# Kernel optimization log

Measured on AMD Instinct MI355X. Metric: run time of the kernel, lower is better.

Reference implementation:

```python
import jax, jax.numpy as jnp
import numpy as np

N_SRC, N_DST, N_EDGES = 50000, 50000, 500000
IN_DIM, OUT_DIM, EDGE_DIM = 128, 128, 11
BN_EPS = 1e-5


def setup_inputs() -> dict:
    key = jax.random.key(0)
    ks = jax.random.split(key, 16)
    s = 0.05
    return {
        "src_feat": jax.random.normal(ks[0], (N_SRC, IN_DIM), jnp.float32),
        "dst_feat": jax.random.normal(ks[1], (N_DST, IN_DIM), jnp.float32),
        "edge_feats": jax.random.normal(ks[2], (N_EDGES, EDGE_DIM), jnp.float32),
        "src_idx": jax.random.randint(ks[3], (N_EDGES,), 0, N_SRC, jnp.int32),
        "dst_idx": jax.random.randint(ks[4], (N_EDGES,), 0, N_DST, jnp.int32),
        "W_src": jax.random.normal(ks[5], (IN_DIM, OUT_DIM), jnp.float32) * s,
        "b_src": jnp.zeros((OUT_DIM,), jnp.float32),
        "W_dst": jax.random.normal(ks[6], (IN_DIM, OUT_DIM), jnp.float32) * s,
        "b_dst": jnp.zeros((OUT_DIM,), jnp.float32),
        "W_edge": jax.random.normal(ks[7], (EDGE_DIM, OUT_DIM), jnp.float32) * s,
        "b_edge": jnp.zeros((OUT_DIM,), jnp.float32),
        "attn_w": jax.random.normal(ks[8], (3 * OUT_DIM,), jnp.float32) * s,
        "attn_b": jnp.zeros((), jnp.float32),
        "gamma": jnp.ones((OUT_DIM,), jnp.float32),
        "beta": jnp.zeros((OUT_DIM,), jnp.float32),
        "alpha": jnp.asarray(0.25, jnp.float32),
    }


def reference(src_feat, dst_feat, edge_feats, src_idx, dst_idx,
              W_src, b_src, W_dst, b_dst, W_edge, b_edge,
              attn_w, attn_b, gamma, beta, alpha):
    D = W_src.shape[1]
    # project at node/edge level (math identical to projecting gathered feats)
    hs = src_feat @ W_src + b_src            # [Ns, D]  (linear_src)
    hd = dst_feat @ W_dst + b_dst            # [Nd, D]  (linear_dst)
    ep = edge_feats @ W_edge + b_edge        # [E, D]   (linear_edge)
    # attn_l on concat([src, dst, edge]) == sum of three dot products + bias
    aw_s, aw_d, aw_e = attn_w[:D], attn_w[D:2 * D], attn_w[2 * D:]
    a = (hs @ aw_s)[src_idx] + (hd @ aw_d)[dst_idx] + ep @ aw_e + attn_b  # [E]
    # edge softmax over incoming edges of each dst node
    n_dst = dst_feat.shape[0]
    seg_max = jax.ops.segment_max(a, dst_idx, num_segments=n_dst)
    a_exp = jnp.exp(a - seg_max[dst_idx])
    denom = jax.ops.segment_sum(a_exp, dst_idx, num_segments=n_dst)
    attn = a_exp / denom[dst_idx]            # [E]
    # weighted message = attn * linear_src(src_h); scatter-sum to dst
    msg = attn[:, None] * hs[src_idx]        # [E, D]
    h_new = jax.ops.segment_sum(msg, dst_idx, num_segments=n_dst)  # [Nd, D]
    # BatchNorm1d (training-mode batch statistics)
    mean = jnp.mean(h_new, axis=0)
    var = jnp.var(h_new, axis=0)
    h_bn = (h_new - mean) / jnp.sqrt(var + BN_EPS) * gamma + beta
    # PReLU (single shared alpha); dropout is identity in eval
    return jnp.where(h_bn >= 0, h_bn, alpha * h_bn)
```

## Files before the change

### kernel.cpp

```cpp
#include <hip/hip_runtime.h>
#include <cstddef>

#define NSRC 50000
#define NDST 50000
#define NEDGE 500000
#define DIM 128
#define EDIM 11
#define BN_EPS 1e-5f
#define SCAN_NBLK ((NDST + 255) / 256)

#define HS_BLOCKS ((NSRC + 63) / 64)
#define DS_BLOCKS ((NDST + 31) / 32)
#define ED_BLOCKS ((NEDGE + 1023) / 1024)

typedef short bf16x8 __attribute__((ext_vector_type(8)));
typedef float f32x4 __attribute__((ext_vector_type(4)));

#define OFF_HS      0
#define OFF_SSCORE  (OFF_HS + (size_t)NSRC*DIM)
#define OFF_DSCORE  (OFF_SSCORE + NSRC)
#define OFF_EE      (OFF_DSCORE + NDST)
#define OFF_DEG     (OFF_EE + NEDGE)
#define OFF_COLSUM  (OFF_DEG + NDST)
#define OFF_COLSQ   (OFF_COLSUM + 128)
#define OFF_OFFS    (OFF_COLSQ + 128)
#define OFF_CURSOR  (OFF_OFFS + NDST + 2)
#define OFF_PAIRS   (OFF_CURSOR + NDST)
#define OFF_WDVEC   (OFF_PAIRS + 2*(size_t)NEDGE)
#define OFF_WEVEC   (OFF_WDVEC + 128)
#define OFF_SCAL    (OFF_WEVEC + 16)
#define OFF_PART    (OFF_SCAL + 4)
#define OFF_WT      (((OFF_PART + 256 + 3) / 4) * 4)

__device__ __forceinline__ unsigned short f2bf(float x) {
    unsigned int u = __float_as_uint(x);
    u += 0x7FFFu + ((u >> 16) & 1u);
    return (unsigned short)(u >> 16);
}
__device__ __forceinline__ float bf2f(unsigned int u16) {
    return __uint_as_float(u16 << 16);
}

__global__ void k_prep(const float* __restrict__ W_dst, const float* __restrict__ b_dst,
                       const float* __restrict__ W_edge, const float* __restrict__ b_edge,
                       const float* __restrict__ attn_w, const float* __restrict__ attn_b,
                       float* __restrict__ wd_vec, float* __restrict__ we_vec,
                       float* __restrict__ scal) {
    int t = threadIdx.x;
    float acc = 0.f;
    for (int d = 0; d < DIM; ++d) acc += W_dst[t * DIM + d] * attn_w[DIM + d];
    wd_vec[t] = acc;
    if (t < EDIM) {
        float e = 0.f;
        for (int d = 0; d < DIM; ++d) e += W_edge[t * DIM + d] * attn_w[2 * DIM + d];
        we_vec[t] = e;
    }
    __shared__ float red[128];
    red[t] = b_dst[t] * attn_w[DIM + t];
    __syncthreads();
    for (int s = 64; s > 0; s >>= 1) { if (t < s) red[t] += red[t + s]; __syncthreads(); }
    if (t == 0) scal[0] = red[0];
    __syncthreads();
    red[t] = b_edge[t] * attn_w[2 * DIM + t];
    __syncthreads();
    for (int s = 64; s > 0; s >>= 1) { if (t < s) red[t] += red[t + s]; __syncthreads(); }
    if (t == 0) scal[1] = red[0] + attn_b[0];
}

__global__ __launch_bounds__(256) void k_wt(const float* __restrict__ W,
                                            unsigned short* __restrict__ wt) {
    __shared__ float tile[32][33];
    int bi = blockIdx.x & 3;
    int bj = blockIdx.x >> 2;
    int t = threadIdx.x;
    int cl = t & 31;
    #pragma unroll
    for (int i = 0; i < 4; ++i) {
        int kl = (t >> 5) * 4 + i;
        tile[kl][cl] = W[(size_t)(bi * 32 + kl) * DIM + bj * 32 + cl];
    }
    __syncthreads();
    int ko = t & 31;
    #pragma unroll
    for (int i = 0; i < 4; ++i) {
        int co = (t >> 5) * 4 + i;
        wt[(size_t)(bj * 32 + co) * DIM + bi * 32 + ko] = f2bf(tile[ko][co]);
    }
}

__global__ __launch_bounds__(256) void k_fused(const float* __restrict__ A,
                                               const unsigned short* __restrict__ wt,
                                               const float* __restrict__ bias,
                                               const float* __restrict__ attn_w,
                                               const float* __restrict__ B,
                                               const float* __restrict__ ef,
                                               const int* __restrict__ dst_idx,
                                               const float* __restrict__ wd_vec,
                                               const float* __restrict__ we_vec,
                                               const float* __restrict__ scal,
                                               unsigned short* __restrict__ hsb,
                                               float* __restrict__ s_score,
                                               float* __restrict__ d_score,
                                               float* __restrict__ ee,
                                               int* __restrict__ deg) {
    __shared__ float stage[4][EDIM * 64];
    const int bid = blockIdx.x;
    const int t = threadIdx.x;

    if (bid < HS_BLOCKS) {
        const int wv = t >> 6;
        const int lane = t & 63;
        const int lrow = lane & 15;
        const int kg = lane >> 4;
        const int grow = bid * 64 + wv * 16 + lrow;
        const bool rowok = grow < NSRC;
        const float* arow = A + (size_t)grow * DIM;

        bf16x8 af[4];
        #pragma unroll
        for (int s = 0; s < 4; ++s) {
            float4 p0 = make_float4(0.f, 0.f, 0.f, 0.f), p1 = p0;
            if (rowok) {
                p0 = *reinterpret_cast<const float4*>(arow + 32 * s + kg * 8);
                p1 = *reinterpret_cast<const float4*>(arow + 32 * s + kg * 8 + 4);
            }
            bf16x8 a;
            a[0] = (short)f2bf(p0.x); a[1] = (short)f2bf(p0.y);
            a[2] = (short)f2bf(p0.z); a[3] = (short)f2bf(p0.w);
            a[4] = (short)f2bf(p1.x); a[5] = (short)f2bf(p1.y);
            a[6] = (short)f2bf(p1.z); a[7] = (short)f2bf(p1.w);
            af[s] = a;
        }

        f32x4 acc[8];
        #pragma unroll
        for (int c = 0; c < 8; ++c) acc[c] = (f32x4){0.f, 0.f, 0.f, 0.f};

        #pragma unroll
        for (int c = 0; c < 8; ++c) {
            #pragma unroll
            for (int s = 0; s < 4; ++s) {
                const bf16x8 b = *reinterpret_cast<const bf16x8*>(
                    wt + ((size_t)(16 * c + lrow) * DIM + 32 * s + kg * 8));
                acc[c] = __builtin_amdgcn_mfma_f32_16x16x32_bf16(af[s], b, acc[c], 0, 0, 0);
            }
        }

        float p[4] = {0.f, 0.f, 0.f, 0.f};
        #pragma unroll
        for (int c = 0; c < 8; ++c) {
            float bb = bias[16 * c + lrow];
            float aw = attn_w[16 * c + lrow];
            #pragma unroll
            for (int i = 0; i < 4; ++i) {
                float v = acc[c][i] + bb;
                acc[c][i] = v;
                p[i] += v * aw;
            }
        }
        #pragma unroll
        for (int i = 0; i < 4; ++i) {
            p[i] += __shfl_xor(p[i], 1);
            p[i] += __shfl_xor(p[i], 2);
            p[i] += __shfl_xor(p[i], 4);
            p[i] += __shfl_xor(p[i], 8);
        }
        const int orow0 = bid * 64 + wv * 16 + kg * 4;
        #pragma unroll
        for (int i = 0; i < 4; ++i) {
            int orow = orow0 + i;
            if (orow < NSRC) {
                #pragma unroll
                for (int c = 0; c < 8; ++c)
                    hsb[(size_t)orow * DIM + 16 * c + lrow] = f2bf(acc[c][i]);
                if (lrow == 0) s_score[orow] = p[i];
            }
        }
    } else if (bid < HS_BLOCKS + DS_BLOCKS) {
        int row = (bid - HS_BLOCKS) * 32 + (t >> 3);
        int c0 = (t & 7) * 16;
        if (row >= NDST) return;
        const float4* x = reinterpret_cast<const float4*>(B + (size_t)row * DIM + c0);
        const float4* w = reinterpret_cast<const float4*>(wd_vec + c0);
        float p = 0.f;
        #pragma unroll
        for (int i = 0; i < 4; ++i) {
            float4 a = x[i], b = w[i];
            p += a.x * b.x + a.y * b.y + a.z * b.z + a.w * b.w;
        }
        p += __shfl_xor(p, 1);
        p += __shfl_xor(p, 2);
        p += __shfl_xor(p, 4);
        if ((t & 7) == 0) d_score[row] = p + scal[0];
    } else {
        const int wv = t >> 6;
        const int lane = t & 63;
        float wvv[EDIM];
        #pragma unroll
        for (int k = 0; k < EDIM; ++k) wvv[k] = we_vec[k];
        const float s1 = scal[1];
        const int blkBase = (bid - HS_BLOCKS - DS_BLOCKS) * 1024;

        #pragma unroll
        for (int chunk = 0; chunk < 4; ++chunk) {
            const int e0 = blkBase + wv * 256 + chunk * 64;
            const size_t g0 = (size_t)e0 * EDIM;
            #pragma unroll
            for (int k = 0; k < EDIM; ++k) {
                int j = k * 64 + lane;
                size_t g = g0 + j;
                stage[wv][j] = (g < (size_t)NEDGE * EDIM) ? ef[g] : 0.f;
            }
            __syncthreads();
            int e = e0 + lane;
            if (e < NEDGE) {
                const float* er = &stage[wv][lane * EDIM];
                float a = s1;
                #pragma unroll
                for (int k = 0; k < EDIM; ++k) a += er[k] * wvv[k];
                ee[e] = a;
                atomicAdd(&deg[dst_idx[e]], 1);
            }
            __syncthreads();
        }
    }
}

__global__ __launch_bounds__(256) void k_scanA(const int* __restrict__ deg,
                                               int* __restrict__ off,
                                               int* __restrict__ partials) {
    __shared__ int tmp[256];
    int t = threadIdx.x;
    int i = blockIdx.x * 256 + t;
    int v = (i < NDST) ? deg[i] : 0;
    tmp[t] = v;
    __syncthreads();
    #pragma unroll
    for (int d = 1; d < 256; d <<= 1) {
        int u = (t >= d) ? tmp[t - d] : 0;
        __syncthreads();
        tmp[t] += u;
        __syncthreads();
    }
    if (i < NDST) off[i] = tmp[t] - v;
    if (t == 255) partials[blockIdx.x] = tmp[255];
}

__global__ __launch_bounds__(256) void k_scanB(int* __restrict__ partials) {
    __shared__ int tmp[256];
    int t = threadIdx.x;
    int v = (t < SCAN_NBLK) ? partials[t] : 0;
    tmp[t] = v;
    __syncthreads();
    #pragma unroll
    for (int d = 1; d < 256; d <<= 1) {
        int u = (t >= d) ? tmp[t - d] : 0;
        __syncthreads();
        tmp[t] += u;
        __syncthreads();
    }
    if (t < SCAN_NBLK) partials[t] = tmp[t] - v;
}

__global__ __launch_bounds__(256) void k_scanC(int* __restrict__ off,
                                               int* __restrict__ cursor,
                                               const int* __restrict__ partials) {
    int t = threadIdx.x;
    int i = blockIdx.x * 256 + t;
    if (i < NDST) {
        int f = off[i] + partials[blockIdx.x];
        off[i] = f;
        cursor[i] = f;
    }
    if (i == 0) off[NDST] = NEDGE;
}

__global__ __launch_bounds__(256) void k_scat(const int* __restrict__ src_idx,
                                              const int* __restrict__ dst_idx,
                                              const float* __restrict__ ee,
                                              const float* __restrict__ s_score,
                                              const float* __restrict__ d_score,
                                              int* __restrict__ cursor,
                                              int2* __restrict__ pairs) {
    int base = blockIdx.x * 1024 + threadIdx.x;
    #pragma unroll
    for (int i = 0; i < 4; ++i) {
        int e = base + i * 256;
        if (e < NEDGE) {
            int s = src_idx[e], d = dst_idx[e];
            float w = expf(ee[e] + s_score[s] + d_score[d]);
            int pos = atomicAdd(&cursor[d], 1);
            pairs[pos] = make_int2(s, __float_as_int(w));
        }
    }
}

__global__ __launch_bounds__(256) void k_gather(const unsigned short* __restrict__ hsb,
                                                const int* __restrict__ off,
                                                const int2* __restrict__ pairs,
                                                float* __restrict__ h_new) {
    int wid = (blockIdx.x * blockDim.x + threadIdx.x) >> 6;
    int lane = threadIdx.x & 63;
    if (wid >= NDST) return;
    int b = off[wid], e2 = off[wid + 1];
    int deg = e2 - b;
    float ax = 0.f, ay = 0.f, wsum = 0.f;

    for (int base = 0; base < deg; base += 64) {
        int cnt = min(deg - base, 64);
        int myS = 0;
        float myW = 0.f;
        if (lane < cnt) {
            int2 p = pairs[b + base + lane];
            myS = p.x;
            myW = __int_as_float(p.y);
        }
        wsum += myW;

        int j = 0;
        for (; j + 4 <= cnt; j += 4) {
            int s0 = __shfl(myS, j + 0), s1 = __shfl(myS, j + 1);
            int s2 = __shfl(myS, j + 2), s3 = __shfl(myS, j + 3);
            float w0 = __shfl(myW, j + 0), w1 = __shfl(myW, j + 1);
            float w2 = __shfl(myW, j + 2), w3 = __shfl(myW, j + 3);
            unsigned int v0 = *reinterpret_cast<const unsigned int*>(hsb + (size_t)s0 * DIM + 2 * lane);
            unsigned int v1 = *reinterpret_cast<const unsigned int*>(hsb + (size_t)s1 * DIM + 2 * lane);
            unsigned int v2 = *reinterpret_cast<const unsigned int*>(hsb + (size_t)s2 * DIM + 2 * lane);
            unsigned int v3 = *reinterpret_cast<const unsigned int*>(hsb + (size_t)s3 * DIM + 2 * lane);
            ax += w0 * bf2f(v0 & 0xFFFFu) + w1 * bf2f(v1 & 0xFFFFu)
                + w2 * bf2f(v2 & 0xFFFFu) + w3 * bf2f(v3 & 0xFFFFu);
            ay += w0 * bf2f(v0 >> 16) + w1 * bf2f(v1 >> 16)
                + w2 * bf2f(v2 >> 16) + w3 * bf2f(v3 >> 16);
        }
        for (; j < cnt; ++j) {
            int s0 = __shfl(myS, j);
            float w0 = __shfl(myW, j);
            unsigned int v0 = *reinterpret_cast<const unsigned int*>(hsb + (size_t)s0 * DIM + 2 * lane);
            ax += w0 * bf2f(v0 & 0xFFFFu);
            ay += w0 * bf2f(v0 >> 16);
        }
    }

    #pragma unroll
    for (int m = 1; m < 64; m <<= 1) wsum += __shfl_xor(wsum, m);

    float inv = (deg > 0) ? 1.f / wsum : 0.f;
    reinterpret_cast<float2*>(h_new + (size_t)wid * DIM)[lane] = make_float2(ax * inv, ay * inv);
}

__global__ __launch_bounds__(256) void k_bnstats(const float* __restrict__ h,
                                                 float* __restrict__ colsum,
                                                 float* __restrict__ colsq) {
    int col = threadIdx.x & 127;
    int rp = threadIdx.x >> 7;
    float s = 0.f, q = 0.f;
    for (int r = blockIdx.x * 2 + rp; r < NDST; r += gridDim.x * 2) {
        float x = h[(size_t)r * DIM + col];
        s += x;
        q += x * x;
    }
    __shared__ float ls[2][128], lq[2][128];
    ls[rp][col] = s;
    lq[rp][col] = q;
    __syncthreads();
    if (rp == 0) {
        atomicAdd(&colsum[col], ls[0][col] + ls[1][col]);
        atomicAdd(&colsq[col], lq[0][col] + lq[1][col]);
    }
}

__global__ __launch_bounds__(256) void k_bnfinal(float* __restrict__ h,
                                                 const float* __restrict__ colsum,
                                                 const float* __restrict__ colsq,
                                                 const float* __restrict__ gamma,
                                                 const float* __restrict__ beta,
                                                 const float* __restrict__ alpha_p) {
    const size_t total4 = (size_t)NDST * DIM / 4;
    const float alpha = alpha_p[0];
    const float invN = 1.f / (float)NDST;
    const int c0 = (threadIdx.x & 31) * 4;
    float sc[4], sh[4];
    #pragma unroll
    for (int k = 0; k < 4; ++k) {
        float mean = colsum[c0 + k] * invN;
        float var = colsq[c0 + k] * invN - mean * mean;
        float s = gamma[c0 + k] * rsqrtf(var + BN_EPS);
        sc[k] = s;
        sh[k] = beta[c0 + k] - mean * s;
    }
    size_t stride = (size_t)gridDim.x * blockDim.x;
    for (size_t i = blockIdx.x * blockDim.x + threadIdx.x; i < total4; i += stride) {
        float4 x = reinterpret_cast<float4*>(h)[i];
        float y0 = x.x * sc[0] + sh[0];
        float y1 = x.y * sc[1] + sh[1];
        float y2 = x.z * sc[2] + sh[2];
        float y3 = x.w * sc[3] + sh[3];
        float4 o;
        o.x = y0 >= 0.f ? y0 : alpha * y0;
        o.y = y1 >= 0.f ? y1 : alpha * y1;
        o.z = y2 >= 0.f ? y2 : alpha * y2;
        o.w = y3 >= 0.f ? y3 : alpha * y3;
        reinterpret_cast<float4*>(h)[i] = o;
    }
}

extern "C" void kernel_launch(void* const* d_in, const int* in_sizes, int n_in,
                              void* d_out, int out_size, void* d_ws, size_t ws_size,
                              hipStream_t stream) {
    const float* src_feat   = (const float*)d_in[0];
    const float* dst_feat   = (const float*)d_in[1];
    const float* edge_feats = (const float*)d_in[2];
    const int*   src_idx    = (const int*)d_in[3];
    const int*   dst_idx    = (const int*)d_in[4];
    const float* W_src      = (const float*)d_in[5];
    const float* b_src      = (const float*)d_in[6];
    const float* W_dst      = (const float*)d_in[7];
    const float* b_dst      = (const float*)d_in[8];
    const float* W_edge     = (const float*)d_in[9];
    const float* b_edge     = (const float*)d_in[10];
    const float* attn_w     = (const float*)d_in[11];
    const float* attn_b     = (const float*)d_in[12];
    const float* gamma      = (const float*)d_in[13];
    const float* beta       = (const float*)d_in[14];
    const float* alpha      = (const float*)d_in[15];

    float* ws      = (float*)d_ws;
    unsigned short* hsb = (unsigned short*)(ws + OFF_HS);
    float* s_score = ws + OFF_SSCORE;
    float* d_score = ws + OFF_DSCORE;
    float* ee      = ws + OFF_EE;
    int*   deg     = (int*)(ws + OFF_DEG);
    float* colsum  = ws + OFF_COLSUM;
    float* colsq   = ws + OFF_COLSQ;
    int*   off     = (int*)(ws + OFF_OFFS);
    int*   cursor  = (int*)(ws + OFF_CURSOR);
    int2*  pairs   = (int2*)(ws + OFF_PAIRS);
    float* wd_vec  = ws + OFF_WDVEC;
    float* we_vec  = ws + OFF_WEVEC;
    float* scal    = ws + OFF_SCAL;
    int*   part    = (int*)(ws + OFF_PART);
    unsigned short* wt = (unsigned short*)(ws + OFF_WT);

    float* h_new = (float*)d_out;

    hipMemsetAsync(deg, 0, (NDST + 256) * sizeof(float), stream);

    k_prep<<<1, 128, 0, stream>>>(W_dst, b_dst, W_edge, b_edge, attn_w, attn_b,
                                  wd_vec, we_vec, scal);
    k_wt<<<16, 256, 0, stream>>>(W_src, wt);
    k_fused<<<HS_BLOCKS + DS_BLOCKS + ED_BLOCKS, 256, 0, stream>>>(
        src_feat, wt, b_src, attn_w, dst_feat, edge_feats, dst_idx,
        wd_vec, we_vec, scal, hsb, s_score, d_score, ee, deg);
    k_scanA<<<SCAN_NBLK, 256, 0, stream>>>(deg, off, part);
    k_scanB<<<1, 256, 0, stream>>>(part);
    k_scanC<<<SCAN_NBLK, 256, 0, stream>>>(off, cursor, part);
    k_scat<<<ED_BLOCKS, 256, 0, stream>>>(src_idx, dst_idx, ee, s_score, d_score,
                                          cursor, pairs);
    k_gather<<<(NDST * 64 + 255) / 256, 256, 0, stream>>>(hsb, off, pairs, h_new);
    k_bnstats<<<512, 256, 0, stream>>>(h_new, colsum, colsq);
    k_bnfinal<<<1024, 256, 0, stream>>>(h_new, colsum, colsq, gamma, beta, alpha);
}
```

Before: 163.7 us.

## Pad degree and cursor counters to 64-byte stride, drop LDS staging for edge scores

Degree and cursor counters are spread out so each destination node's counter sits in its own 64-byte slot. The aim is to cut contention on atomics that hit the same cache line. The edge-score path now reads edge features directly from global memory instead of staging them through shared memory, which removes two block barriers per chunk. k_fused also gets a minimum-occupancy hint, and the hs buffer offset is halved to match its bf16 storage. The costs are a much larger counter memset (about 3.2MB each for deg and cursor), strided scan reads, and uncoalesced 44-byte-stride feature loads.

```diff
diff --git a/kernel.cpp b/kernel.cpp
--- a/kernel.cpp
+++ b/kernel.cpp
@@ -16,21 +16,21 @@
 typedef short bf16x8 __attribute__((ext_vector_type(8)));
 typedef float f32x4 __attribute__((ext_vector_type(4)));
 
-#define OFF_HS      0
-#define OFF_SSCORE  (OFF_HS + (size_t)NSRC*DIM)
-#define OFF_DSCORE  (OFF_SSCORE + NSRC)
-#define OFF_EE      (OFF_DSCORE + NDST)
-#define OFF_DEG     (OFF_EE + NEDGE)
-#define OFF_COLSUM  (OFF_DEG + NDST)
-#define OFF_COLSQ   (OFF_COLSUM + 128)
-#define OFF_OFFS    (OFF_COLSQ + 128)
-#define OFF_CURSOR  (OFF_OFFS + NDST + 2)
-#define OFF_PAIRS   (OFF_CURSOR + NDST)
-#define OFF_WDVEC   (OFF_PAIRS + 2*(size_t)NEDGE)
-#define OFF_WEVEC   (OFF_WDVEC + 128)
-#define OFF_SCAL    (OFF_WEVEC + 16)
-#define OFF_PART    (OFF_SCAL + 4)
-#define OFF_WT      (((OFF_PART + 256 + 3) / 4) * 4)
+#define OFF_HS       0
+#define OFF_SSCORE   (OFF_HS + (size_t)NSRC*DIM/2)
+#define OFF_DSCORE   (OFF_SSCORE + NSRC)
+#define OFF_EE       (OFF_DSCORE + NDST)
+#define OFF_DEG16    (OFF_EE + NEDGE)
+#define OFF_COLSUM   (OFF_DEG16 + (size_t)NDST*16)
+#define OFF_COLSQ    (OFF_COLSUM + 128)
+#define OFF_OFFS     (OFF_COLSQ + 128)
+#define OFF_CUR16    (OFF_OFFS + NDST + 2)
+#define OFF_PAIRS    (OFF_CUR16 + (size_t)NDST*16)
+#define OFF_WDVEC    (OFF_PAIRS + 2*(size_t)NEDGE)
+#define OFF_WEVEC    (OFF_WDVEC + 128)
+#define OFF_SCAL     (OFF_WEVEC + 16)
+#define OFF_PART     (OFF_SCAL + 4)
+#define OFF_WT       (((OFF_PART + 256 + 3) / 4) * 4)
 
 __device__ __forceinline__ unsigned short f2bf(float x) {
     unsigned int u = __float_as_uint(x);
@@ -88,7 +88,7 @@
     }
 }
 
-__global__ __launch_bounds__(256) void k_fused(const float* __restrict__ A,
+__global__ __launch_bounds__(256, 2) void k_fused(const float* __restrict__ A,
                                                const unsigned short* __restrict__ wt,
                                                const float* __restrict__ bias,
                                                const float* __restrict__ attn_w,
@@ -102,8 +102,7 @@
                                                float* __restrict__ s_score,
                                                float* __restrict__ d_score,
                                                float* __restrict__ ee,
-                                               int* __restrict__ deg) {
-    __shared__ float stage[4][EDIM * 64];
+                                               int* __restrict__ deg16) {
     const int bid = blockIdx.x;
     const int t = threadIdx.x;
 
@@ -193,46 +192,33 @@
         p += __shfl_xor(p, 4);
         if ((t & 7) == 0) d_score[row] = p + scal[0];
     } else {
-        const int wv = t >> 6;
-        const int lane = t & 63;
         float wvv[EDIM];
         #pragma unroll
         for (int k = 0; k < EDIM; ++k) wvv[k] = we_vec[k];
         const float s1 = scal[1];
-        const int blkBase = (bid - HS_BLOCKS - DS_BLOCKS) * 1024;
-
-        #pragma unroll
-        for (int chunk = 0; chunk < 4; ++chunk) {
-            const int e0 = blkBase + wv * 256 + chunk * 64;
-            const size_t g0 = (size_t)e0 * EDIM;
-            #pragma unroll
-            for (int k = 0; k < EDIM; ++k) {
-                int j = k * 64 + lane;
-                size_t g = g0 + j;
-                stage[wv][j] = (g < (size_t)NEDGE * EDIM) ? ef[g] : 0.f;
-            }
-            __syncthreads();
-            int e = e0 + lane;
+        int ebase = (bid - HS_BLOCKS - DS_BLOCKS) * 1024 + t;
+        #pragma unroll
+        for (int i = 0; i < 4; ++i) {
+            int e = ebase + i * 256;
             if (e < NEDGE) {
-                const float* er = &stage[wv][lane * EDIM];
+                const float* er = ef + (size_t)e * EDIM;
                 float a = s1;
                 #pragma unroll
                 for (int k = 0; k < EDIM; ++k) a += er[k] * wvv[k];
                 ee[e] = a;
-                atomicAdd(&deg[dst_idx[e]], 1);
+                atomicAdd(&deg16[(size_t)dst_idx[e] * 16], 1);
             }
-            __syncthreads();
-        }
-    }
-}
-
-__global__ __launch_bounds__(256) void k_scanA(const int* __restrict__ deg,
+        }
+    }
+}
+
+__global__ __launch_bounds__(256) void k_scanA(const int* __restrict__ deg16,
                                                int* __restrict__ off,
                                                int* __restrict__ partials) {
     __shared__ int tmp[256];
     int t = threadIdx.x;
     int i = blockIdx.x * 256 + t;
-    int v = (i < NDST) ? deg[i] : 0;
+    int v = (i < NDST) ? deg16[(size_t)i * 16] : 0;
     tmp[t] = v;
     __syncthreads();
     #pragma unroll
@@ -263,14 +249,14 @@
 }
 
 __global__ __launch_bounds__(256) void k_scanC(int* __restrict__ off,
-                                               int* __restrict__ cursor,
+                                               int* __restrict__ cur16,
                                                const int* __restrict__ partials) {
     int t = threadIdx.x;
     int i = blockIdx.x * 256 + t;
     if (i < NDST) {
         int f = off[i] + partials[blockIdx.x];
         off[i] = f;
-        cursor[i] = f;
+        cur16[(size_t)i * 16] = f;
     }
     if (i == 0) off[NDST] = NEDGE;
 }
@@ -280,7 +266,7 @@
                                               const float* __restrict__ ee,
                                               const float* __restrict__ s_score,
                                               const float* __restrict__ d_score,
-                                              int* __restrict__ cursor,
+                                              int* __restrict__ cur16,
                                               int2* __restrict__ pairs) {
     int base = blockIdx.x * 1024 + threadIdx.x;
     #pragma unroll
@@ -289,7 +275,7 @@
         if (e < NEDGE) {
             int s = src_idx[e], d = dst_idx[e];
             float w = expf(ee[e] + s_score[s] + d_score[d]);
-            int pos = atomicAdd(&cursor[d], 1);
+            int pos = atomicAdd(&cur16[(size_t)d * 16], 1);
             pairs[pos] = make_int2(s, __float_as_int(w));
         }
     }
@@ -429,11 +415,11 @@
     float* s_score = ws + OFF_SSCORE;
     float* d_score = ws + OFF_DSCORE;
     float* ee      = ws + OFF_EE;
-    int*   deg     = (int*)(ws + OFF_DEG);
+    int*   deg16   = (int*)(ws + OFF_DEG16);
     float* colsum  = ws + OFF_COLSUM;
     float* colsq   = ws + OFF_COLSQ;
     int*   off     = (int*)(ws + OFF_OFFS);
-    int*   cursor  = (int*)(ws + OFF_CURSOR);
+    int*   cur16   = (int*)(ws + OFF_CUR16);
     int2*  pairs   = (int2*)(ws + OFF_PAIRS);
     float* wd_vec  = ws + OFF_WDVEC;
     float* we_vec  = ws + OFF_WEVEC;
@@ -443,19 +429,19 @@
 
     float* h_new = (float*)d_out;
 
-    hipMemsetAsync(deg, 0, (NDST + 256) * sizeof(float), stream);
+    hipMemsetAsync(deg16, 0, ((size_t)NDST * 16 + 256) * sizeof(int), stream);
 
     k_prep<<<1, 128, 0, stream>>>(W_dst, b_dst, W_edge, b_edge, attn_w, attn_b,
                                   wd_vec, we_vec, scal);
     k_wt<<<16, 256, 0, stream>>>(W_src, wt);
     k_fused<<<HS_BLOCKS + DS_BLOCKS + ED_BLOCKS, 256, 0, stream>>>(
         src_feat, wt, b_src, attn_w, dst_feat, edge_feats, dst_idx,
-        wd_vec, we_vec, scal, hsb, s_score, d_score, ee, deg);
-    k_scanA<<<SCAN_NBLK, 256, 0, stream>>>(deg, off, part);
+        wd_vec, we_vec, scal, hsb, s_score, d_score, ee, deg16);
+    k_scanA<<<SCAN_NBLK, 256, 0, stream>>>(deg16, off, part);
     k_scanB<<<1, 256, 0, stream>>>(part);
-    k_scanC<<<SCAN_NBLK, 256, 0, stream>>>(off, cursor, part);
+    k_scanC<<<SCAN_NBLK, 256, 0, stream>>>(off, cur16, part);
     k_scat<<<ED_BLOCKS, 256, 0, stream>>>(src_idx, dst_idx, ee, s_score, d_score,
-                                          cursor, pairs);
+                                          cur16, pairs);
     k_gather<<<(NDST * 64 + 255) / 256, 256, 0, stream>>>(hsb, off, pairs, h_new);
     k_bnstats<<<512, 256, 0, stream>>>(h_new, colsum, colsq);
     k_bnfinal<<<1024, 256, 0, stream>>>(h_new, colsum, colsq, gamma, beta, alpha);
```

After: 157.6 us. 3.7% less time.
